# Performance work log

Measured on AMD Instinct MI355X. Metric: run time of the kernel, lower is better.

Reference implementation:

```python
import jax, jax.numpy as jnp
import numpy as np

N = 4096      # num nodes (attention sequence length)
D = 256       # input_dim
HID = 256     # hidden_dim
H = 4         # num_heads
HD = D // H   # head_dim = 64
E = 131072    # num edges (avg degree 32)


def setup_inputs() -> dict:
    key = jax.random.key(0)
    ks = jax.random.split(key, 12)
    s = 0.02
    return {
        "x": jax.random.normal(ks[0], (N, D), jnp.float32),
        "edge_index": jax.random.randint(ks[1], (2, E), 0, N, jnp.int32),
        # torch.nn.MultiheadAttention params
        "in_proj_w": jax.random.normal(ks[2], (3 * D, D), jnp.float32) * s,
        "in_proj_b": jnp.zeros((3 * D,), jnp.float32),
        "out_proj_w": jax.random.normal(ks[3], (D, D), jnp.float32) * s,
        "out_proj_b": jnp.zeros((D,), jnp.float32),
        # GCNConv params (PyG Linear weight is [out, in], bias separate)
        "W1": jax.random.normal(ks[4], (HID, D), jnp.float32) * s,
        "b1": jnp.zeros((HID,), jnp.float32),
        "W2": jax.random.normal(ks[5], (HID, HID), jnp.float32) * s,
        "b2": jnp.zeros((HID,), jnp.float32),
    }


def _mha(x, in_proj_w, in_proj_b, out_proj_w, out_proj_b):
    # x: [N, D]; self-attention with nodes as the sequence (batch = 1)
    qkv = x @ in_proj_w.T + in_proj_b            # [N, 3D]
    q, k, v = jnp.split(qkv, 3, axis=-1)
    q = q.reshape(N, H, HD)
    k = k.reshape(N, H, HD)
    v = v.reshape(N, H, HD)
    scores = jnp.einsum('nhd,mhd->hnm', q, k) / jnp.sqrt(jnp.float32(HD))
    attn = jax.nn.softmax(scores, axis=-1)        # [H, N, N]
    out = jnp.einsum('hnm,mhd->nhd', attn, v).reshape(N, D)
    return out @ out_proj_w.T + out_proj_b


def _gcn(x, W, b, src, dst):
    # PyG GCNConv: linear -> add self-loops -> sym deg^{-1/2} norm -> scatter-add
    h = x @ W.T                                   # [N, out]
    loop = jnp.arange(N, dtype=src.dtype)
    src2 = jnp.concatenate([src, loop])
    dst2 = jnp.concatenate([dst, loop])
    deg = jax.ops.segment_sum(jnp.ones_like(dst2, jnp.float32), dst2, num_segments=N)
    dinv = jnp.where(deg > 0, jax.lax.rsqrt(deg), 0.0)
    norm = dinv[src2] * dinv[dst2]                # [E+N]
    msg = h[src2] * norm[:, None]
    out = jax.ops.segment_sum(msg, dst2, num_segments=N)
    return out + b


def reference(x, edge_index, in_proj_w, in_proj_b, out_proj_w, out_proj_b, W1, b1, W2, b2):
    src, dst = edge_index[0], edge_index[1]
    h = _mha(x, in_proj_w, in_proj_b, out_proj_w, out_proj_b)
    h = _gcn(h, W1, b1, src, dst)
    h = jax.nn.relu(h)
    h = _gcn(h, W2, b2, src, dst)
    return h
```

## Files before the change

### kernel.cpp

```cpp
#include <hip/hip_runtime.h>
#include <math.h>

#define NN   4096
#define DD   256
#define NHD  768
#define NH   4
#define NE   131072
#define KVSPLIT 4
#define PAD  128
#define QSCALE 0.18033688011112042f

using bfx8   = __attribute__((ext_vector_type(8))) short;
using f32x4  = __attribute__((ext_vector_type(4))) float;
using f32x16 = __attribute__((ext_vector_type(16))) float;
#define MFMA16(a,b,c) __builtin_amdgcn_mfma_f32_16x16x32_bf16(a, b, c, 0, 0, 0)
#define MFMA32(a,b,c) __builtin_amdgcn_mfma_f32_32x32x16_bf16(a, b, c, 0, 0, 0)

__device__ __forceinline__ ushort bf16_rne(float f) {
  uint u = __float_as_uint(f);
  u += 0x7fffu + ((u >> 16) & 1u);
  return (ushort)(u >> 16);
}
__device__ __forceinline__ float bf16_tof(ushort h) {
  return __uint_as_float(((uint)h) << 16);
}
__device__ __forceinline__ float fexp2(float x) { return __builtin_amdgcn_exp2f(x); }
__device__ __forceinline__ int swzf(int row) {
  return ((row & 7) << 2) ^ ((row & 8) << 1);
}
__device__ __forceinline__ uint4 cvt8(const float* f) {
  ushort hs[8];
#pragma unroll
  for (int j = 0; j < 8; ++j) hs[j] = bf16_rne(f[j]);
  return make_uint4((uint)hs[0] | ((uint)hs[1] << 16), (uint)hs[2] | ((uint)hs[3] << 16),
                    (uint)hs[4] | ((uint)hs[5] << 16), (uint)hs[6] | ((uint)hs[7] << 16));
}

__global__ __launch_bounds__(256, 4) void gemmm(
    const ushort* __restrict__ Ah, const ushort* __restrict__ Wh,
    const float* __restrict__ bias, float* __restrict__ Cf,
    ushort* __restrict__ Cb,
    int M, int Nc, int K, float preScale, int preScaleCols,
    int mode, ushort* __restrict__ kout, ushort* __restrict__ vout) {
  __shared__ uint sAh[2048], sBh[2048];
  const int tid = threadIdx.x;
  const int wid = tid >> 6, lane = tid & 63;
  const int m15 = lane & 15, g2 = lane >> 4;
  const int wr = wid >> 1, wc = wid & 1;
  const int mb = blockIdx.x << 6, nb = blockIdx.y << 6;
  const int sw = swzf(m15);
  const int pr0 = tid >> 3, pc0 = (tid & 7) << 2;
  const int pr1 = (tid + 256) >> 3;
  const int wi0 = (pr0 << 5) + (pc0 ^ swzf(pr0));
  const int wi1 = (pr1 << 5) + (pc0 ^ swzf(pr1));
  uint4 ra0, ra1, rb0, rb1;
  auto issue = [&](int k0) {
    ra0 = *(const uint4*)(Ah + (size_t)(mb + pr0) * K + k0 + (pc0 << 1));
    ra1 = *(const uint4*)(Ah + (size_t)(mb + pr1) * K + k0 + (pc0 << 1));
    rb0 = *(const uint4*)(Wh + (size_t)(nb + pr0) * K + k0 + (pc0 << 1));
    rb1 = *(const uint4*)(Wh + (size_t)(nb + pr1) * K + k0 + (pc0 << 1));
  };
  f32x4 acc[2][2];
#pragma unroll
  for (int r = 0; r < 2; ++r)
#pragma unroll
    for (int c = 0; c < 2; ++c) acc[r][c] = (f32x4){0.f, 0.f, 0.f, 0.f};

  issue(0);
  for (int k0 = 0; k0 < K; k0 += 64) {
    __syncthreads();
    *(uint4*)&sAh[wi0] = ra0; *(uint4*)&sBh[wi0] = rb0;
    *(uint4*)&sAh[wi1] = ra1; *(uint4*)&sBh[wi1] = rb1;
    __syncthreads();
    if (k0 + 64 < K) issue(k0 + 64);
#pragma unroll
    for (int c = 0; c < 2; ++c) {
      bfx8 ah[2], bh[2];
#pragma unroll
      for (int r = 0; r < 2; ++r) {
        int rowA = (wr << 5) + (r << 4) + m15;
        ah[r] = __builtin_bit_cast(bfx8, *(const uint4*)&sAh[(rowA << 5) + (((c << 4) + (g2 << 2)) ^ sw)]);
        int rowB = (wc << 5) + (r << 4) + m15;
        bh[r] = __builtin_bit_cast(bfx8, *(const uint4*)&sBh[(rowB << 5) + (((c << 4) + (g2 << 2)) ^ sw)]);
      }
#pragma unroll
      for (int r = 0; r < 2; ++r)
#pragma unroll
        for (int cc = 0; cc < 2; ++cc)
          acc[r][cc] = MFMA16(ah[r], bh[cc], acc[r][cc]);
    }
  }
#pragma unroll
  for (int r = 0; r < 2; ++r)
#pragma unroll
    for (int cc = 0; cc < 2; ++cc) {
      int col = nb + (wc << 5) + (cc << 4) + m15;
      float bv = bias ? bias[col] : 0.f;
      float sc = (col < preScaleCols) ? preScale : 1.f;
      int row0 = mb + (wr << 5) + (r << 4) + (g2 << 2);
      float v4[4];
#pragma unroll
      for (int j = 0; j < 4; ++j) v4[j] = (acc[r][cc][j] + bv) * sc;
      if (mode == 1) {
        if (col < 256) {
#pragma unroll
          for (int j = 0; j < 4; ++j)
            Cb[(size_t)(row0 + j) * 256 + col] = bf16_rne(v4[j]);
        } else if (col < 512) {
#pragma unroll
          for (int j = 0; j < 4; ++j)
            kout[(size_t)(row0 + j) * 256 + (col - 256)] = bf16_rne(v4[j]);
        } else {
          ushort4 vs = make_ushort4(bf16_rne(v4[0]), bf16_rne(v4[1]),
                                    bf16_rne(v4[2]), bf16_rne(v4[3]));
          *(ushort4*)(vout + ((size_t)(col - 512) << 12) + row0) = vs;
        }
      } else {
#pragma unroll
        for (int j = 0; j < 4; ++j) {
          int row = row0 + j;
          if (Cf) Cf[(size_t)row * Nc + col] = v4[j];
          if (Cb) Cb[(size_t)row * Nc + col] = bf16_rne(v4[j]);
        }
      }
    }
}

__global__ __launch_bounds__(256) void k_cvt(
    const float* __restrict__ x, const float* __restrict__ ipw,
    const float* __restrict__ opw, const float* __restrict__ W1,
    const float* __restrict__ W2, const float* __restrict__ opb,
    ushort* xh, ushort* iph, ushort* w1h, ushort* w2h,
    ushort* opth, float* bfv, int* cnt, int* cursor) {
  __shared__ float sT[64 * 65];
  int b = blockIdx.x;
  if (b >= 672) {
    if (b < 688) {
      int tx = b - 672, by = tx >> 2, bx = tx & 3;
      int r = threadIdx.x >> 2, cb = (threadIdx.x & 3) << 4;
      const float* src = opw + (size_t)(by * 64 + r) * 256 + bx * 64 + cb;
#pragma unroll
      for (int i = 0; i < 4; ++i) {
        float4 v = *(const float4*)(src + i * 4);
        sT[r * 65 + cb + i * 4 + 0] = v.x; sT[r * 65 + cb + i * 4 + 1] = v.y;
        sT[r * 65 + cb + i * 4 + 2] = v.z; sT[r * 65 + cb + i * 4 + 3] = v.w;
      }
      __syncthreads();
      int d = threadIdx.x >> 2, nb2 = (threadIdx.x & 3) << 4;
      float f[16];
#pragma unroll
      for (int i = 0; i < 16; ++i) f[i] = sT[(nb2 + i) * 65 + d];
      size_t o = (size_t)(bx * 64 + d) * 256 + by * 64 + nb2;
      *(uint4*)(opth + o)     = cvt8(&f[0]);
      *(uint4*)(opth + o + 8) = cvt8(&f[8]);
    } else if (b == 688) {
      int t = threadIdx.x;
      sT[t] = opb[t];
      __syncthreads();
      float acc = 0.f;
      const float* wr = W1 + (size_t)t * 256;
      for (int k = 0; k < 256; ++k) acc += wr[k] * sT[k];
      bfv[t] = acc;
    } else {
      int i = ((b - 689) * 256 + threadIdx.x) * 4;
      *(int4*)(cnt + i) = make_int4(0, 0, 0, 0);
      *(int4*)(cursor + i) = make_int4(0, 0, 0, 0);
    }
    return;
  }
  const float* src; ushort* hi; int base;
  if (b < 512)      { src = x;   hi = xh;  base = b; }
  else if (b < 608) { src = ipw; hi = iph; base = b - 512; }
  else if (b < 640) { src = W1;  hi = w1h; base = b - 608; }
  else              { src = W2;  hi = w2h; base = b - 640; }
  size_t i = (size_t)base * 256 + threadIdx.x;
  float f[8];
  *(float4*)&f[0] = *(const float4*)(src + i * 8);
  *(float4*)&f[4] = *(const float4*)(src + i * 8 + 4);
  *(uint4*)(hi + i * 8) = cvt8(f);
}

__global__ void k_hist(const int* __restrict__ dst, int* __restrict__ cnt) {
  int e = blockIdx.x * 256 + threadIdx.x;
  if (e < NE) atomicAdd(&cnt[dst[e]], 1);
}

__global__ __launch_bounds__(256, 2) void flashm(
    const ushort* __restrict__ qhg, const ushort* __restrict__ khg,
    const ushort* __restrict__ vhg,
    float* __restrict__ opT, float* __restrict__ ml) {
  __shared__ uint sKh[2048], sVh[2048];

  const int b = blockIdx.x;
  const int id = b & 15;
  const int h = id >> 2, split = id & 3;
  const int qb = (b >> 4) << 7;
  const int kv0 = split << 10;
  const int NT = 16;

  const int tid = threadIdx.x;
  const int wid = tid >> 6, lane = tid & 63;
  const int m31 = lane & 31, g = lane >> 5;

  bfx8 qh[4];
  {
    const size_t qoff = (size_t)(qb + (wid << 5) + m31) * 256 + h * 64 + (g << 3);
#pragma unroll
    for (int c = 0; c < 4; ++c)
      qh[c] = __builtin_bit_cast(bfx8, *(const uint4*)(qhg + qoff + (c << 4)));
  }

  f32x16 o[2];
#pragma unroll
  for (int dt = 0; dt < 2; ++dt)
#pragma unroll
    for (int j = 0; j < 16; ++j) o[dt][j] = 0.f;
  float mreg = -1e30f;
  float lacc[16];
#pragma unroll
  for (int j = 0; j < 16; ++j) lacc[j] = 0.f;

  const int pr0 = tid >> 3, pc0 = (tid & 7) << 2;
  const int pr1 = (tid + 256) >> 3;
  const int wi0 = (pr0 << 5) + (pc0 ^ swzf(pr0));
  const int wi1 = (pr1 << 5) + (pc0 ^ swzf(pr1));
  uint4 rk0, rk1, rv0, rv1;
  auto issue = [&](int kv) {
    rk0 = *(const uint4*)(khg + (size_t)(kv + pr0) * 256 + h * 64 + (pc0 << 1));
    rk1 = *(const uint4*)(khg + (size_t)(kv + pr1) * 256 + h * 64 + (pc0 << 1));
    rv0 = *(const uint4*)(vhg + ((size_t)(h * 64 + pr0) << 12) + kv + (pc0 << 1));
    rv1 = *(const uint4*)(vhg + ((size_t)(h * 64 + pr1) << 12) + kv + (pc0 << 1));
  };

  issue(kv0);
  for (int it = 0; it < NT; ++it) {
    __syncthreads();
    *(uint4*)&sKh[wi0] = rk0; *(uint4*)&sVh[wi0] = rv0;
    *(uint4*)&sKh[wi1] = rk1; *(uint4*)&sVh[wi1] = rv1;
    __syncthreads();
    if (it + 1 < NT) issue(kv0 + ((it + 1) << 6));

    f32x16 s[2];
#pragma unroll
    for (int kt = 0; kt < 2; ++kt) {
#pragma unroll
      for (int j = 0; j < 16; ++j) s[kt][j] = 0.f;
      const int row = (kt << 5) + m31;
      const int rb = row << 5;
      const int sw2 = swzf(row);
      __builtin_amdgcn_s_setprio(1);
#pragma unroll
      for (int c = 0; c < 4; ++c) {
        int col = ((c << 3) + (g << 2)) ^ sw2;
        bfx8 kh = __builtin_bit_cast(bfx8, *(const uint4*)&sKh[rb + col]);
        s[kt] = MFMA32(kh, qh[c], s[kt]);
      }
      __builtin_amdgcn_s_setprio(0);
    }

    float v16[16];
#pragma unroll
    for (int j = 0; j < 16; ++j) v16[j] = fmaxf(s[0][j], s[1][j]);
#pragma unroll
    for (int st = 8; st; st >>= 1)
#pragma unroll
      for (int j = 0; j < 8; ++j)
        if (j < st) v16[j] = fmaxf(v16[j], v16[j + st]);
    float mt = fmaxf(v16[0], __shfl_xor(v16[0], 32));
    int need = (mt > mreg + 8.f) ? 1 : 0;
    if (__any(need)) {
      float mn = fmaxf(mreg, mt);
      float al = fexp2(mreg - mn);
      mreg = mn;
#pragma unroll
      for (int j = 0; j < 16; ++j) lacc[j] *= al;
#pragma unroll
      for (int dt = 0; dt < 2; ++dt)
#pragma unroll
        for (int j = 0; j < 16; ++j) o[dt][j] *= al;
    }
    float p0[16], p1[16];
#pragma unroll
    for (int j = 0; j < 16; ++j) {
      p0[j] = fexp2(s[0][j] - mreg);
      p1[j] = fexp2(s[1][j] - mreg);
      lacc[j] += p0[j] + p1[j];
    }

    uint puh[2][8];
#pragma unroll
    for (int kt = 0; kt < 2; ++kt)
#pragma unroll
      for (int jj = 0; jj < 8; ++jj) {
        float a = kt ? p1[2 * jj] : p0[2 * jj];
        float bq = kt ? p1[2 * jj + 1] : p0[2 * jj + 1];
        puh[kt][jj] = (__float_as_uint(a) >> 16) | (__float_as_uint(bq) & 0xffff0000u);
      }

#pragma unroll
    for (int dt = 0; dt < 2; ++dt) {
      const int row = (dt << 5) + m31;
      const int rb = row << 5;
      const int sw2 = swzf(row);
      __builtin_amdgcn_s_setprio(1);
#pragma unroll
      for (int kt = 0; kt < 2; ++kt)
#pragma unroll
        for (int cc = 0; cc < 2; ++cc) {
          int cA = ((kt << 4) + (cc << 3) + (g << 1)) ^ sw2;
          int cB = ((kt << 4) + (cc << 3) + (g << 1) + 4) ^ sw2;
          uint2 vh0 = *(const uint2*)&sVh[rb + cA];
          uint2 vh1 = *(const uint2*)&sVh[rb + cB];
          bfx8 ah = __builtin_bit_cast(bfx8, make_uint4(vh0.x, vh0.y, vh1.x, vh1.y));
          bfx8 bh = __builtin_bit_cast(bfx8, make_uint4(puh[kt][4 * cc], puh[kt][4 * cc + 1],
                                                        puh[kt][4 * cc + 2], puh[kt][4 * cc + 3]));
          o[dt] = MFMA32(ah, bh, o[dt]);
        }
      __builtin_amdgcn_s_setprio(0);
    }
  }

  float lreg;
  {
#pragma unroll
    for (int st = 8; st; st >>= 1)
#pragma unroll
      for (int j = 0; j < 8; ++j)
        if (j < st) lacc[j] += lacc[j + st];
    lreg = lacc[0] + __shfl_xor(lacc[0], 32);
  }

  const int region = (split * NH + h) * (NN >> 5) + (qb >> 5) + wid;
  float* ob = opT + (size_t)region * 2048;
#pragma unroll
  for (int dt = 0; dt < 2; ++dt)
#pragma unroll
    for (int r = 0; r < 16; ++r) {
      int d = (dt << 5) + (r & 3) + ((r >> 2) << 3) + (g << 2);
      ob[(d << 5) + m31] = o[dt][r];
    }
  if (!g) {
    size_t qi = (size_t)(split * NH + h) * NN + qb + (wid << 5) + m31;
    ml[qi * 2]     = mreg;
    ml[qi * 2 + 1] = lreg;
  }
}

__global__ __launch_bounds__(256) void k_comb(const float* __restrict__ opT,
    const float* __restrict__ ml, ushort* __restrict__ attnh) {
  int qt = blockIdx.x, h = blockIdx.y, t = threadIdx.x;
  int qq = t & 31, dg = t >> 5;
  int q = (qt << 5) + qq;
  float ms[KVSPLIT], ls[KVSPLIT];
#pragma unroll
  for (int s = 0; s < KVSPLIT; ++s) {
    const float* e = ml + ((size_t)(s * NH + h) * NN + q) * 2;
    ms[s] = e[0]; ls[s] = e[1];
  }
  float Mx = ms[0];
#pragma unroll
  for (int s = 1; s < KVSPLIT; ++s) Mx = fmaxf(Mx, ms[s]);
  float cs[KVSPLIT], L = 0.f;
#pragma unroll
  for (int s = 0; s < KVSPLIT; ++s) { cs[s] = fexp2(ms[s] - Mx); L += ls[s] * cs[s]; }
  float invL = 1.f / L;
  float vals[8];
#pragma unroll
  for (int j = 0; j < 8; ++j) {
    int d = (dg << 3) + j;
    float acc = 0.f;
#pragma unroll
    for (int s = 0; s < KVSPLIT; ++s)
      acc += opT[((size_t)((s * NH + h) * (NN >> 5) + qt)) * 2048 + (d << 5) + qq] * cs[s];
    vals[j] = acc * invL;
  }
  size_t oo = (size_t)q * DD + h * 64 + (dg << 3);
  *(uint4*)(attnh + oo) = cvt8(vals);
}

__global__ void k_fill(const int* __restrict__ src, const int* __restrict__ dst,
    const int* __restrict__ cnt, int* cursor, int* __restrict__ lst,
    float* __restrict__ dinv) {
  int e = blockIdx.x * 256 + threadIdx.x;
  if (e < NN) dinv[e] = (float)(1.0 / sqrt((double)(cnt[e] + 1)));
  if (e < NE) {
    int d = dst[e];
    int pos = atomicAdd(&cursor[d], 1);
    if (pos < PAD) lst[(d << 7) + pos] = src[e];
  }
}
__device__ __forceinline__ float4 bf4_tof(ushort4 u) {
  return make_float4(bf16_tof(u.x), bf16_tof(u.y), bf16_tof(u.z), bf16_tof(u.w));
}
__global__ __launch_bounds__(256) void k_gather(const ushort* __restrict__ hin,
    const int* __restrict__ cnt, const int* __restrict__ lst,
    const float* __restrict__ dinv, const float* __restrict__ bias,
    float* __restrict__ outF, ushort* __restrict__ oh, int relu) {
  int g = (blockIdx.x << 2) + (threadIdx.x >> 6);
  int lane = threadIdx.x & 63;
  float di = dinv[g];
  int c4 = lane << 2;
  float4 hv = bf4_tof(*(const ushort4*)(hin + (size_t)g * DD + c4));
  float w = di * di;
  float a0x = hv.x * w, a0y = hv.y * w, a0z = hv.z * w, a0w = hv.w * w;
  float a1x = 0, a1y = 0, a1z = 0, a1w = 0;
  float a2x = 0, a2y = 0, a2z = 0, a2w = 0;
  float a3x = 0, a3y = 0, a3z = 0, a3w = 0;
  int num = min(cnt[g], PAD);
  const int* lrow = lst + (g << 7);
  int i = 0;
  for (; i + 4 <= num; i += 4) {
    int4 s4 = *(const int4*)(lrow + i);
    float w0 = dinv[s4.x] * di, w1 = dinv[s4.y] * di;
    float w2 = dinv[s4.z] * di, w3 = dinv[s4.w] * di;
    float4 h0 = bf4_tof(*(const ushort4*)(hin + (size_t)s4.x * DD + c4));
    float4 h1 = bf4_tof(*(const ushort4*)(hin + (size_t)s4.y * DD + c4));
    float4 h2 = bf4_tof(*(const ushort4*)(hin + (size_t)s4.z * DD + c4));
    float4 h3 = bf4_tof(*(const ushort4*)(hin + (size_t)s4.w * DD + c4));
    a0x += h0.x * w0; a0y += h0.y * w0; a0z += h0.z * w0; a0w += h0.w * w0;
    a1x += h1.x * w1; a1y += h1.y * w1; a1z += h1.z * w1; a1w += h1.w * w1;
    a2x += h2.x * w2; a2y += h2.y * w2; a2z += h2.z * w2; a2w += h2.w * w2;
    a3x += h3.x * w3; a3y += h3.y * w3; a3z += h3.z * w3; a3w += h3.w * w3;
  }
  for (; i < num; ++i) {
    int sI = lrow[i];
    float ww = dinv[sI] * di;
    float4 hs = bf4_tof(*(const ushort4*)(hin + (size_t)sI * DD + c4));
    a0x += hs.x * ww; a0y += hs.y * ww; a0z += hs.z * ww; a0w += hs.w * ww;
  }
  float4 bv = *(const float4*)(bias + c4);
  float4 acc = make_float4((a0x + a1x) + (a2x + a3x) + bv.x,
                           (a0y + a1y) + (a2y + a3y) + bv.y,
                           (a0z + a1z) + (a2z + a3z) + bv.z,
                           (a0w + a1w) + (a2w + a3w) + bv.w);
  if (relu) {
    acc.x = fmaxf(acc.x, 0.f); acc.y = fmaxf(acc.y, 0.f);
    acc.z = fmaxf(acc.z, 0.f); acc.w = fmaxf(acc.w, 0.f);
  }
  if (outF) *(float4*)(outF + (size_t)g * DD + c4) = acc;
  if (oh) {
    size_t oo = (size_t)g * DD + c4;
    *(ushort4*)(oh + oo) = make_ushort4(bf16_rne(acc.x), bf16_rne(acc.y),
                                        bf16_rne(acc.z), bf16_rne(acc.w));
  }
}

extern "C" void kernel_launch(void* const* d_in, const int* in_sizes, int n_in,
                              void* d_out, int out_size, void* d_ws, size_t ws_size,
                              hipStream_t stream) {
  const float* x   = (const float*)d_in[0];
  const int*   ei  = (const int*)d_in[1];
  const float* ipw = (const float*)d_in[2];
  const float* ipb = (const float*)d_in[3];
  const float* opw = (const float*)d_in[4];
  const float* opb = (const float*)d_in[5];
  const float* W1  = (const float*)d_in[6];
  const float* b1  = (const float*)d_in[7];
  const float* W2  = (const float*)d_in[8];
  const float* b2  = (const float*)d_in[9];
  const int* srcI = ei;
  const int* dstI = ei + NE;

  char* w = (char*)d_ws;
  ushort* qhg   = (ushort*)w; w += (size_t)NN * DD * 2;
  ushort* khg   = (ushort*)w; w += (size_t)NN * DD * 2;
  ushort* vhg   = (ushort*)w; w += (size_t)NH * NN * 64 * 2;
  ushort* xh    = (ushort*)w; w += (size_t)NN * DD * 2;
  ushort* iph   = (ushort*)w; w += (size_t)NHD * DD * 2;
  ushort* w1h   = (ushort*)w; w += (size_t)DD * DD * 2;
  ushort* w2h   = (ushort*)w; w += (size_t)DD * DD * 2;
  ushort* opth  = (ushort*)w; w += (size_t)DD * DD * 2;
  ushort* wfh   = (ushort*)w; w += (size_t)DD * DD * 2;
  float*  bfv   = (float*)w;  w += (size_t)DD * 4;
  ushort* hlin1 = (ushort*)w; w += (size_t)NN * DD * 2;
  ushort* hlin2 = (ushort*)w; w += (size_t)NN * DD * 2;
  ushort* g1h   = (ushort*)w; w += (size_t)NN * DD * 2;
  float*  opT   = (float*)w;  w += (size_t)KVSPLIT * NH * NN * 64 * 4;
  float*  ml    = (float*)w;  w += (size_t)KVSPLIT * NH * NN * 2 * 4;
  int*    cnt    = (int*)w;   w += NN * 4;
  int*    cursor = (int*)w;   w += NN * 4;
  float*  dinv   = (float*)w; w += NN * 4;
  int*    lst    = (int*)w;   w += (size_t)NN * PAD * 4;
  ushort* attnh = xh;

  hipLaunchKernelGGL(k_cvt, dim3(693), dim3(256), 0, stream,
                     x, ipw, opw, W1, W2, opb,
                     xh, iph, w1h, w2h, opth, bfv, cnt, cursor);
  hipLaunchKernelGGL(k_hist, dim3(NE / 256), dim3(256), 0, stream, dstI, cnt);
  hipLaunchKernelGGL(k_fill, dim3(NE / 256), dim3(256), 0, stream, srcI, dstI, cnt,
                     cursor, lst, dinv);

  hipLaunchKernelGGL(gemmm, dim3(4, 4), dim3(256), 0, stream,
                     w1h, opth, (const float*)nullptr, (float*)nullptr, wfh,
                     DD, DD, DD, 1.f, 0, 0, (ushort*)nullptr, (ushort*)nullptr);

  hipLaunchKernelGGL(gemmm, dim3(64, 12), dim3(256), 0, stream,
                     xh, iph, ipb, (float*)nullptr, qhg,
                     NN, NHD, DD, QSCALE, DD, 1, khg, vhg);
  hipLaunchKernelGGL(flashm, dim3((NN / 128) * 16), dim3(256), 0, stream,
                     qhg, khg, vhg, opT, ml);
  hipLaunchKernelGGL(k_comb, dim3(NN / 32, NH), dim3(256), 0, stream, opT, ml, attnh);

  hipLaunchKernelGGL(gemmm, dim3(64, 4), dim3(256), 0, stream,
                     attnh, wfh, bfv, (float*)nullptr, hlin1,
                     NN, DD, DD, 1.f, 0, 0, (ushort*)nullptr, (ushort*)nullptr);
  hipLaunchKernelGGL(k_gather, dim3(NN / 4), dim3(256), 0, stream, hlin1, cnt, lst,
                     dinv, b1, (float*)nullptr, g1h, 1);
  hipLaunchKernelGGL(gemmm, dim3(64, 4), dim3(256), 0, stream,
                     g1h, w2h, (const float*)nullptr, (float*)nullptr, hlin2,
                     NN, DD, DD, 1.f, 0, 0, (ushort*)nullptr, (ushort*)nullptr);
  hipLaunchKernelGGL(k_gather, dim3(NN / 4), dim3(256), 0, stream, hlin2, cnt, lst,
                     dinv, b2, (float*)d_out, (ushort*)nullptr, 0);
}
```

Before: 113.5 us.

## Double-buffer flash attention K/V tiles and merge degree histogram into fill kernel

The flash attention kernel now keeps two LDS buffers for K/V tiles and prefetches two tiles ahead. This leaves one barrier per iteration instead of two, so global loads overlap with MFMA work. Separately, the histogram kernel and dinv array are removed: the atomic cursor from the fill pass serves as the degree, and gather computes rsqrt(deg+1) on the fly. The cost is doubled LDS use per block, which may limit occupancy, plus extra degree loads and rsqrt in the gather loops.

```diff
diff --git a/kernel.cpp b/kernel.cpp
--- a/kernel.cpp
+++ b/kernel.cpp
@@ -131,7 +131,7 @@
     const float* __restrict__ opw, const float* __restrict__ W1,
     const float* __restrict__ W2, const float* __restrict__ opb,
     ushort* xh, ushort* iph, ushort* w1h, ushort* w2h,
-    ushort* opth, float* bfv, int* cnt, int* cursor) {
+    ushort* opth, float* bfv, int* cursor) {
   __shared__ float sT[64 * 65];
   int b = blockIdx.x;
   if (b >= 672) {
@@ -163,7 +163,6 @@
       bfv[t] = acc;
     } else {
       int i = ((b - 689) * 256 + threadIdx.x) * 4;
-      *(int4*)(cnt + i) = make_int4(0, 0, 0, 0);
       *(int4*)(cursor + i) = make_int4(0, 0, 0, 0);
     }
     return;
@@ -180,16 +179,21 @@
   *(uint4*)(hi + i * 8) = cvt8(f);
 }
 
-__global__ void k_hist(const int* __restrict__ dst, int* __restrict__ cnt) {
+__global__ void k_fill(const int* __restrict__ src, const int* __restrict__ dst,
+    int* cursor, int* __restrict__ lst) {
   int e = blockIdx.x * 256 + threadIdx.x;
-  if (e < NE) atomicAdd(&cnt[dst[e]], 1);
+  if (e < NE) {
+    int d = dst[e];
+    int pos = atomicAdd(&cursor[d], 1);
+    if (pos < PAD) lst[(d << 7) + pos] = src[e];
+  }
 }
 
 __global__ __launch_bounds__(256, 2) void flashm(
     const ushort* __restrict__ qhg, const ushort* __restrict__ khg,
     const ushort* __restrict__ vhg,
     float* __restrict__ opT, float* __restrict__ ml) {
-  __shared__ uint sKh[2048], sVh[2048];
+  __shared__ uint sKh[4096], sVh[4096];
 
   const int b = blockIdx.x;
   const int id = b & 15;
@@ -231,14 +235,24 @@
     rv0 = *(const uint4*)(vhg + ((size_t)(h * 64 + pr0) << 12) + kv + (pc0 << 1));
     rv1 = *(const uint4*)(vhg + ((size_t)(h * 64 + pr1) << 12) + kv + (pc0 << 1));
   };
+  auto writebuf = [&](int buf) {
+    uint* K = sKh + (buf << 11);
+    uint* V = sVh + (buf << 11);
+    *(uint4*)&K[wi0] = rk0; *(uint4*)&V[wi0] = rv0;
+    *(uint4*)&K[wi1] = rk1; *(uint4*)&V[wi1] = rv1;
+  };
 
   issue(kv0);
+  writebuf(0);
+  issue(kv0 + 64);
+  __syncthreads();
+
   for (int it = 0; it < NT; ++it) {
-    __syncthreads();
-    *(uint4*)&sKh[wi0] = rk0; *(uint4*)&sVh[wi0] = rv0;
-    *(uint4*)&sKh[wi1] = rk1; *(uint4*)&sVh[wi1] = rv1;
-    __syncthreads();
-    if (it + 1 < NT) issue(kv0 + ((it + 1) << 6));
+    const int cur = it & 1;
+    if (it + 1 < NT) writebuf(cur ^ 1);
+    if (it + 2 < NT) issue(kv0 + ((it + 2) << 6));
+    const uint* Kb = sKh + (cur << 11);
+    const uint* Vb = sVh + (cur << 11);
 
     f32x16 s[2];
 #pragma unroll
@@ -252,7 +266,7 @@
 #pragma unroll
       for (int c = 0; c < 4; ++c) {
         int col = ((c << 3) + (g << 2)) ^ sw2;
-        bfx8 kh = __builtin_bit_cast(bfx8, *(const uint4*)&sKh[rb + col]);
+        bfx8 kh = __builtin_bit_cast(bfx8, *(const uint4*)&Kb[rb + col]);
         s[kt] = MFMA32(kh, qh[c], s[kt]);
       }
       __builtin_amdgcn_s_setprio(0);
@@ -309,8 +323,8 @@
         for (int cc = 0; cc < 2; ++cc) {
           int cA = ((kt << 4) + (cc << 3) + (g << 1)) ^ sw2;
           int cB = ((kt << 4) + (cc << 3) + (g << 1) + 4) ^ sw2;
-          uint2 vh0 = *(const uint2*)&sVh[rb + cA];
-          uint2 vh1 = *(const uint2*)&sVh[rb + cB];
+          uint2 vh0 = *(const uint2*)&Vb[rb + cA];
+          uint2 vh1 = *(const uint2*)&Vb[rb + cB];
           bfx8 ah = __builtin_bit_cast(bfx8, make_uint4(vh0.x, vh0.y, vh1.x, vh1.y));
           bfx8 bh = __builtin_bit_cast(bfx8, make_uint4(puh[kt][4 * cc], puh[kt][4 * cc + 1],
                                                         puh[kt][4 * cc + 2], puh[kt][4 * cc + 3]));
@@ -318,6 +332,7 @@
         }
       __builtin_amdgcn_s_setprio(0);
     }
+    __syncthreads();
   }
 
   float lreg;
@@ -378,27 +393,18 @@
   *(uint4*)(attnh + oo) = cvt8(vals);
 }
 
-__global__ void k_fill(const int* __restrict__ src, const int* __restrict__ dst,
-    const int* __restrict__ cnt, int* cursor, int* __restrict__ lst,
-    float* __restrict__ dinv) {
-  int e = blockIdx.x * 256 + threadIdx.x;
-  if (e < NN) dinv[e] = (float)(1.0 / sqrt((double)(cnt[e] + 1)));
-  if (e < NE) {
-    int d = dst[e];
-    int pos = atomicAdd(&cursor[d], 1);
-    if (pos < PAD) lst[(d << 7) + pos] = src[e];
-  }
-}
 __device__ __forceinline__ float4 bf4_tof(ushort4 u) {
   return make_float4(bf16_tof(u.x), bf16_tof(u.y), bf16_tof(u.z), bf16_tof(u.w));
 }
+__device__ __forceinline__ float drs(int d) { return rsqrtf((float)(d + 1)); }
 __global__ __launch_bounds__(256) void k_gather(const ushort* __restrict__ hin,
-    const int* __restrict__ cnt, const int* __restrict__ lst,
-    const float* __restrict__ dinv, const float* __restrict__ bias,
+    const int* __restrict__ deg, const int* __restrict__ lst,
+    const float* __restrict__ bias,
     float* __restrict__ outF, ushort* __restrict__ oh, int relu) {
   int g = (blockIdx.x << 2) + (threadIdx.x >> 6);
   int lane = threadIdx.x & 63;
-  float di = dinv[g];
+  int dg = deg[g];
+  float di = drs(dg);
   int c4 = lane << 2;
   float4 hv = bf4_tof(*(const ushort4*)(hin + (size_t)g * DD + c4));
   float w = di * di;
@@ -406,13 +412,13 @@
   float a1x = 0, a1y = 0, a1z = 0, a1w = 0;
   float a2x = 0, a2y = 0, a2z = 0, a2w = 0;
   float a3x = 0, a3y = 0, a3z = 0, a3w = 0;
-  int num = min(cnt[g], PAD);
+  int num = min(dg, PAD);
   const int* lrow = lst + (g << 7);
   int i = 0;
   for (; i + 4 <= num; i += 4) {
     int4 s4 = *(const int4*)(lrow + i);
-    float w0 = dinv[s4.x] * di, w1 = dinv[s4.y] * di;
-    float w2 = dinv[s4.z] * di, w3 = dinv[s4.w] * di;
+    float w0 = drs(deg[s4.x]) * di, w1 = drs(deg[s4.y]) * di;
+    float w2 = drs(deg[s4.z]) * di, w3 = drs(deg[s4.w]) * di;
     float4 h0 = bf4_tof(*(const ushort4*)(hin + (size_t)s4.x * DD + c4));
     float4 h1 = bf4_tof(*(const ushort4*)(hin + (size_t)s4.y * DD + c4));
     float4 h2 = bf4_tof(*(const ushort4*)(hin + (size_t)s4.z * DD + c4));
@@ -424,7 +430,7 @@
   }
   for (; i < num; ++i) {
     int sI = lrow[i];
-    float ww = dinv[sI] * di;
+    float ww = drs(deg[sI]) * di;
     float4 hs = bf4_tof(*(const ushort4*)(hin + (size_t)sI * DD + c4));
     a0x += hs.x * ww; a0y += hs.y * ww; a0z += hs.z * ww; a0w += hs.w * ww;
   }
@@ -477,18 +483,15 @@
   ushort* g1h   = (ushort*)w; w += (size_t)NN * DD * 2;
   float*  opT   = (float*)w;  w += (size_t)KVSPLIT * NH * NN * 64 * 4;
   float*  ml    = (float*)w;  w += (size_t)KVSPLIT * NH * NN * 2 * 4;
-  int*    cnt    = (int*)w;   w += NN * 4;
   int*    cursor = (int*)w;   w += NN * 4;
-  float*  dinv   = (float*)w; w += NN * 4;
   int*    lst    = (int*)w;   w += (size_t)NN * PAD * 4;
   ushort* attnh = xh;
 
   hipLaunchKernelGGL(k_cvt, dim3(693), dim3(256), 0, stream,
                      x, ipw, opw, W1, W2, opb,
-                     xh, iph, w1h, w2h, opth, bfv, cnt, cursor);
-  hipLaunchKernelGGL(k_hist, dim3(NE / 256), dim3(256), 0, stream, dstI, cnt);
-  hipLaunchKernelGGL(k_fill, dim3(NE / 256), dim3(256), 0, stream, srcI, dstI, cnt,
-                     cursor, lst, dinv);
+                     xh, iph, w1h, w2h, opth, bfv, cursor);
+  hipLaunchKernelGGL(k_fill, dim3(NE / 256), dim3(256), 0, stream, srcI, dstI,
+                     cursor, lst);
 
   hipLaunchKernelGGL(gemmm, dim3(4, 4), dim3(256), 0, stream,
                      w1h, opth, (const float*)nullptr, (float*)nullptr, wfh,
@@ -504,11 +507,11 @@
   hipLaunchKernelGGL(gemmm, dim3(64, 4), dim3(256), 0, stream,
                      attnh, wfh, bfv, (float*)nullptr, hlin1,
                      NN, DD, DD, 1.f, 0, 0, (ushort*)nullptr, (ushort*)nullptr);
-  hipLaunchKernelGGL(k_gather, dim3(NN / 4), dim3(256), 0, stream, hlin1, cnt, lst,
-                     dinv, b1, (float*)nullptr, g1h, 1);
+  hipLaunchKernelGGL(k_gather, dim3(NN / 4), dim3(256), 0, stream, hlin1, cursor, lst,
+                     b1, (float*)nullptr, g1h, 1);
   hipLaunchKernelGGL(gemmm, dim3(64, 4), dim3(256), 0, stream,
                      g1h, w2h, (const float*)nullptr, (float*)nullptr, hlin2,
                      NN, DD, DD, 1.f, 0, 0, (ushort*)nullptr, (ushort*)nullptr);
-  hipLaunchKernelGGL(k_gather, dim3(NN / 4), dim3(256), 0, stream, hlin2, cnt, lst,
-                     dinv, b2, (float*)d_out, (ushort*)nullptr, 0);
-}
+  hipLaunchKernelGGL(k_gather, dim3(NN / 4), dim3(256), 0, stream, hlin2, cursor, lst,
+                     b2, (float*)d_out, (ushort*)nullptr, 0);
+}
```

Result: faster. 104.5 us (-7.9%).
